# Performance work log

Hardware: AMD Instinct MI355X
Metric: run time of the kernel (lower is better)

The kernel has to match this reference:

```python
import jax, jax.numpy as jnp
import numpy as np


def conv2d(x, w, b):
    # x: [B,C,H,W], w: [O,C,K,K] (VALID, stride 1)
    out = jax.lax.conv_general_dilated(
        x, w, window_strides=(1, 1), padding='VALID',
        dimension_numbers=('NCHW', 'OIHW', 'NCHW'))
    return out + b[None, :, None, None]


def deform_conv2d(x, offset, w, b):
    # torchvision DeformConv2d semantics, offset_groups=1, stride=1, padding=0.
    # x: [B,C,H,W]; offset: [B, 2*K*K, Ho, Wo] with (dy, dx) interleaved per tap.
    B, C, H, W = x.shape
    O, _, K, _ = w.shape
    KK = K * K
    Ho, Wo = H - K + 1, W - K + 1
    off = offset.reshape(B, KK, 2, Ho, Wo)
    ky = (jnp.arange(KK) // K).astype(x.dtype)
    kx = (jnp.arange(KK) % K).astype(x.dtype)
    # sampling positions p0 + p_k + dp  -> [B, KK, Ho, Wo]
    py = ky[None, :, None, None] + jnp.arange(Ho, dtype=x.dtype)[None, None, :, None] + off[:, :, 0]
    px = kx[None, :, None, None] + jnp.arange(Wo, dtype=x.dtype)[None, None, None, :] + off[:, :, 1]
    y0 = jnp.floor(py)
    x0 = jnp.floor(px)
    wy = py - y0  # fractional parts
    wx = px - x0
    y0i = y0.astype(jnp.int32)
    x0i = x0.astype(jnp.int32)

    def corner(yi, xi):
        valid = ((yi >= 0) & (yi < H) & (xi >= 0) & (xi < W)).astype(x.dtype)
        yc = jnp.clip(yi, 0, H - 1)
        xc = jnp.clip(xi, 0, W - 1)
        # per-batch gather over all channels -> [B, C, KK, Ho, Wo]
        g = jax.vmap(lambda im, a, bb: im[:, a, bb])(x, yc, xc)
        return g * valid[:, None]

    v00 = corner(y0i, x0i)
    v01 = corner(y0i, x0i + 1)
    v10 = corner(y0i + 1, x0i)
    v11 = corner(y0i + 1, x0i + 1)
    wy_ = wy[:, None]  # [B,1,KK,Ho,Wo]
    wx_ = wx[:, None]
    samp = (v00 * (1 - wy_) * (1 - wx_) + v01 * (1 - wy_) * wx_
            + v10 * wy_ * (1 - wx_) + v11 * wy_ * wx_)
    out = jnp.einsum('bckhw,ock->bohw', samp, w.reshape(O, C, KK))
    return out + b[None, :, None, None]


_STAGES = [
    # (in_ch, out_ch, K)
    (1, 16, 3), (16, 32, 3), (32, 16, 5), (16, 16, 7), (16, 8, 5), (8, 4, 3),
]


def setup_inputs() -> dict:
    key = jax.random.key(0)
    keys = iter(jax.random.split(key, 64))
    inp = {'x': jax.random.normal(next(keys), (512, 1, 33, 33), dtype=jnp.float32)}
    for i, (ci, co, k) in enumerate(_STAGES, start=1):
        # offset-predicting conv: small init so offsets stay near the regular grid
        inp[f'ow{i}'] = jax.random.normal(next(keys), (2 * k * k, ci, k, k), dtype=jnp.float32) * 0.05
        inp[f'ob{i}'] = jax.random.normal(next(keys), (2 * k * k,), dtype=jnp.float32) * 0.05
        scale = 1.0 / np.sqrt(ci * k * k)
        inp[f'w{i}'] = jax.random.normal(next(keys), (co, ci, k, k), dtype=jnp.float32) * scale
        inp[f'b{i}'] = jax.random.normal(next(keys), (co,), dtype=jnp.float32) * scale
    inp['fc1_w'] = jax.random.normal(next(keys), (256, 13 * 13 * 4), dtype=jnp.float32) * (1.0 / np.sqrt(676))
    inp['fc1_b'] = jnp.zeros((256,), dtype=jnp.float32)
    inp['fc2_w'] = jax.random.normal(next(keys), (10, 256), dtype=jnp.float32) * (1.0 / np.sqrt(256))
    inp['fc2_b'] = jnp.zeros((10,), dtype=jnp.float32)
    return inp


def reference(x, ow1, ob1, w1, b1, ow2, ob2, w2, b2, ow3, ob3, w3, b3,
              ow4, ob4, w4, b4, ow5, ob5, w5, b5, ow6, ob6, w6, b6,
              fc1_w, fc1_b, fc2_w, fc2_b):
    h = jax.nn.relu(deform_conv2d(x, conv2d(x, ow1, ob1), w1, b1))
    h = jax.nn.relu(deform_conv2d(h, conv2d(h, ow2, ob2), w2, b2))
    h = deform_conv2d(h, conv2d(h, ow3, ob3), w3, b3)  # NOTE: no ReLU on stage 3 (matches source)
    h = jax.nn.relu(deform_conv2d(h, conv2d(h, ow4, ob4), w4, b4))
    h = jax.nn.relu(deform_conv2d(h, conv2d(h, ow5, ob5), w5, b5))
    h = jax.nn.relu(deform_conv2d(h, conv2d(h, ow6, ob6), w6, b6))
    flat = h.reshape(h.shape[0], -1)  # [B, 4*13*13]
    z = jax.nn.relu(flat @ fc1_w.T + fc1_b)
    return z @ fc2_w.T + fc2_b
```

## Files before the change

kernel.cpp:

```cpp
#include <hip/hip_runtime.h>

typedef __attribute__((ext_vector_type(8))) short bf16x8;
typedef __attribute__((ext_vector_type(4))) float f32x4;
typedef __attribute__((ext_vector_type(4))) unsigned int u32x4;
typedef unsigned short ushort_t;

__device__ inline ushort_t bf16_trunc(float f) { return (ushort_t)(__float_as_uint(f) >> 16); }
__device__ inline float bf16_to_f(ushort_t u) { return __uint_as_float(((unsigned int)u) << 16); }

__device__ inline unsigned int hi_pair(unsigned int u1, unsigned int u0) {
    return __builtin_amdgcn_perm(u1, u0, 0x07060302u);
}

__device__ inline void split8(const f32x4 sA, const f32x4 sB, bf16x8& ahi, bf16x8& alo)
{
    unsigned int u[8], h[8], d[8];
#pragma unroll
    for (int j = 0; j < 4; ++j) {
        u[j]     = __float_as_uint(sA[j]);
        u[4 + j] = __float_as_uint(sB[j]);
    }
#pragma unroll
    for (int j = 0; j < 8; ++j) {
        h[j] = u[j] & 0xffff0000u;
        d[j] = __float_as_uint(__uint_as_float(u[j]) - __uint_as_float(h[j]));
    }
    union { u32x4 w; bf16x8 v; } H, L;
    H.w = (u32x4){hi_pair(h[1], h[0]), hi_pair(h[3], h[2]), hi_pair(h[5], h[4]), hi_pair(h[7], h[6])};
    L.w = (u32x4){hi_pair(d[1], d[0]), hi_pair(d[3], d[2]), hi_pair(d[5], d[4]), hi_pair(d[7], d[6])};
    ahi = H.v;
    alo = L.v;
}

template<int CI, int KK, int KKPAD, int NPAD, int OC>
__global__ __launch_bounds__(256)
void wprep(const float* __restrict__ w, ushort_t* __restrict__ bhi, ushort_t* __restrict__ blo)
{
    const int idx = blockIdx.x * 256 + threadIdx.x;
    if (idx >= KKPAD * NPAD * CI) return;
    const int kk  = idx / (NPAD * CI);
    const int rem = idx - kk * (NPAD * CI);
    const int n   = rem / CI;
    const int ci  = rem - n * CI;
    const float v = (kk < KK && n < OC) ? w[((size_t)n * CI + ci) * KK + kk] : 0.f;
    const ushort_t h = bf16_trunc(v);
    bhi[idx] = h;
    blo[idx] = bf16_trunc(v - bf16_to_f(h));
}

template<int CI, int KK, int TPAD, int NPAD, int OC>
__global__ __launch_bounds__(256)
void wprep_d(const float* __restrict__ w, ushort_t* __restrict__ bhi, ushort_t* __restrict__ blo)
{
    constexpr int NPASS = (CI + 7) / 8;
    constexpr int TOTAL = NPASS * TPAD * NPAD * 8;
    const int idx = blockIdx.x * 256 + threadIdx.x;
    if (idx >= TOTAL) return;
    const int j     = idx & 7;
    const int n     = (idx >> 3) % NPAD;
    const int kslot = (idx >> 3) / NPAD;
    const int pass  = kslot / TPAD;
    const int tap   = kslot - pass * TPAD;
    const int ci    = pass * 8 + j;
    const float v = (tap < KK && n < OC && ci < CI) ? w[((size_t)n * CI + ci) * KK + tap] : 0.f;
    const ushort_t h = bf16_trunc(v);
    bhi[idx] = h;
    blo[idx] = bf16_trunc(v - bf16_to_f(h));
}

template<int CI, int K, int H, int W, int Ho, int Wo, int OC, int NTTOT, int NT0, int KSTEPS>
__global__ __launch_bounds__(256)
void conv_mfma(const ushort_t* __restrict__ Xhi, const ushort_t* __restrict__ Xlo,
               const ushort_t* __restrict__ Bhi, const ushort_t* __restrict__ Blo,
               const float* __restrict__ bias, float* __restrict__ out, int Mtotal)
{
    constexpr int NPAD = NTTOT * 16;
    constexpr int HW   = H * W;
    constexpr int HoWo = Ho * Wo;
    constexpr int NPASS = CI / 8;
    constexpr int TKS  = 32 / CI;
    constexpr int ROWS = TKS * NT0 * 16;
    constexpr int BSTR = CI + 8;
    constexpr int CH8  = CI / 8;
    constexpr int CHUNKS = ROWS * CH8;

    __shared__ __align__(16) ushort_t sBh[2][ROWS * BSTR];
    __shared__ __align__(16) ushort_t sBl[2][ROWS * BSTR];

    const int tid  = threadIdx.x;
    const int lane = tid & 63;
    const int wid  = tid >> 6;
    const int col  = lane & 15;
    const int quad = lane >> 4;

    const int mBase  = blockIdx.x * 256 + wid * 64;
    const int ntBase = blockIdx.y * NT0;

    int aBase[4];
#pragma unroll
    for (int mt = 0; mt < 4; ++mt) {
        int mm = mBase + mt * 16 + col;
        if (mm >= Mtotal) mm = Mtotal - 1;
        const int b   = mm / HoWo;
        const int pos = mm - b * HoWo;
        const int oy  = pos / Wo;
        const int ox  = pos - oy * Wo;
        aBase[mt] = b * NPASS * HW + oy * W + ox;
    }

    f32x4 acc[4][NT0];
#pragma unroll
    for (int mt = 0; mt < 4; ++mt)
#pragma unroll
        for (int nt = 0; nt < NT0; ++nt) acc[mt][nt] = (f32x4){0.f, 0.f, 0.f, 0.f};

    auto loadSlab = [&](int ks, int buf) {
        const int tap0 = ks * TKS;
        for (int i = tid; i < CHUNKS; i += 256) {
            const int row = i / CH8;
            const int c8  = i - row * CH8;
            const int t   = row / (NT0 * 16);
            const int nn  = row - t * (NT0 * 16);
            int n = ntBase * 16 + nn;
            if (n > NPAD - 1) n = NPAD - 1;
            const int g = ((tap0 + t) * NPAD + n) * CI + c8 * 8;
            *(bf16x8*)(sBh[buf] + row * BSTR + c8 * 8) = *(const bf16x8*)(Bhi + g);
            *(bf16x8*)(sBl[buf] + row * BSTR + c8 * 8) = *(const bf16x8*)(Blo + g);
        }
    };

    loadSlab(0, 0);
    __syncthreads();

#pragma unroll
    for (int ks = 0; ks < KSTEPS; ++ks) {
        if (ks + 1 < KSTEPS) loadSlab(ks + 1, (ks + 1) & 1);

        const int k0   = ks * 32 + quad * 8;
        const int tap  = k0 / CI;
        const int tloc = tap - ks * TKS;
        const int ci   = k0 - tap * CI;
        const int g    = ci >> 3;
        const int dkk  = (tap / K) * W + (tap - (tap / K) * K);

        bf16x8 ah[4], al[4];
#pragma unroll
        for (int mt = 0; mt < 4; ++mt) {
            const size_t aoff = (size_t)(aBase[mt] + g * HW + dkk) * 8;
            ah[mt] = *(const bf16x8*)(Xhi + aoff);
            al[mt] = *(const bf16x8*)(Xlo + aoff);
        }
        const ushort_t* __restrict__ bhp = sBh[ks & 1];
        const ushort_t* __restrict__ blp = sBl[ks & 1];
#pragma unroll
        for (int nt = 0; nt < NT0; ++nt) {
            const int ntg = ntBase + nt;
            if (ntg < NTTOT) {
                const int lrow = ((tloc * NT0 + nt) * 16 + col) * BSTR + ci;
                const bf16x8 bh = *(const bf16x8*)(bhp + lrow);
                const bf16x8 bl = *(const bf16x8*)(blp + lrow);
#pragma unroll
                for (int mt = 0; mt < 4; ++mt) {
                    acc[mt][nt] = __builtin_amdgcn_mfma_f32_16x16x32_bf16(ah[mt], bh, acc[mt][nt], 0, 0, 0);
                    acc[mt][nt] = __builtin_amdgcn_mfma_f32_16x16x32_bf16(al[mt], bh, acc[mt][nt], 0, 0, 0);
                    acc[mt][nt] = __builtin_amdgcn_mfma_f32_16x16x32_bf16(ah[mt], bl, acc[mt][nt], 0, 0, 0);
                }
            }
        }
        __syncthreads();
    }

#pragma unroll
    for (int mt = 0; mt < 4; ++mt) {
#pragma unroll
        for (int nt = 0; nt < NT0; ++nt) {
            const int ntg = ntBase + nt;
            const int n   = ntg * 16 + col;
            if (ntg < NTTOT && n < OC) {
                const float bv = bias[n];
#pragma unroll
                for (int r = 0; r < 4; ++r) {
                    const int m = mBase + mt * 16 + quad * 4 + r;
                    if (m < Mtotal) {
                        const int b   = m / HoWo;
                        const int pos = m - b * HoWo;
                        out[((size_t)b * OC + n) * HoWo + pos] = acc[mt][nt][r] + bv;
                    }
                }
            }
        }
    }
}

template<int K, int CI, int CO, int H, int W, int Ho, int Wo, bool RELU,
         int MT, int TPAD, bool OUTPL>
__global__ __launch_bounds__(MT * 64, 4)
void deform_mfma(const ushort_t* __restrict__ Xhi, const ushort_t* __restrict__ Xlo,
                 const float* __restrict__ off,
                 const ushort_t* __restrict__ Bph, const ushort_t* __restrict__ Bpl,
                 const float* __restrict__ bias,
                 float* __restrict__ outF, ushort_t* __restrict__ oHi, ushort_t* __restrict__ oLo)
{
    static_assert(CI % 16 == 0, "deform_mfma v2 stages 16 channels per pass");
    constexpr int KK     = K * K;
    constexpr int HW     = H * W;
    constexpr int HoWo   = Ho * Wo;
    constexpr int NG8    = CI / 8;
    constexpr int NPASS  = CI / 16;
    constexpr int NPO    = CO / 8;
    constexpr int NT     = (CO + 15) / 16;
    constexpr int NPAD   = NT * 16;
    constexpr int TSTR   = 20;
    constexpr int TG     = TPAD / 4;
    constexpr int nMB    = (HoWo + MT * 16 - 1) / (MT * 16);
    constexpr int THREADS = MT * 64;
    __shared__ __align__(16) float tile[HW * TSTR];

    const int b    = blockIdx.x / nMB;
    const int mb   = blockIdx.x - b * nMB;
    const int tid  = threadIdx.x;
    const int wid  = tid >> 6;
    const int lane = tid & 63;
    const int col  = lane & 15;
    const int quad = lane >> 4;

    const int pixel0 = (mb * MT + wid) * 16;
    const int s      = pixel0 + col;
    const bool am    = (s < HoWo);
    const int oy = s / Wo, ox = s - oy * Wo;

    const float* offB = off + (size_t)b * 2 * KK * HoWo;

    f32x4 acc[NT];
#pragma unroll
    for (int nt = 0; nt < NT; ++nt) acc[nt] = (f32x4){0.f, 0.f, 0.f, 0.f};

    float pw00[TG], pw01[TG], pw10[TG], pw11[TG];
    int   pi00[TG], pi01[TG], pi10[TG], pi11[TG];
    if constexpr (NPASS > 1) {
#pragma unroll
        for (int t = 0; t < TG; ++t) {
            pw00[t] = pw01[t] = pw10[t] = pw11[t] = 0.f;
            pi00[t] = pi01[t] = pi10[t] = pi11[t] = 0;
        }
    }

#pragma unroll
    for (int pass = 0; pass < NPASS; ++pass) {
        __syncthreads();
        for (int pos = tid; pos < HW; pos += THREADS) {
            const size_t gbase = ((size_t)(b * NG8 + pass * 2) * HW + pos) * 8;
            const bf16x8 h0 = *(const bf16x8*)(Xhi + gbase);
            const bf16x8 l0 = *(const bf16x8*)(Xlo + gbase);
            const bf16x8 h1 = *(const bf16x8*)(Xhi + gbase + (size_t)HW * 8);
            const bf16x8 l1 = *(const bf16x8*)(Xlo + gbase + (size_t)HW * 8);
            f32x4 v0, v1, v2, v3;
#pragma unroll
            for (int j = 0; j < 4; ++j) {
                v0[j] = bf16_to_f((ushort_t)h0[j])     + bf16_to_f((ushort_t)l0[j]);
                v1[j] = bf16_to_f((ushort_t)h0[4 + j]) + bf16_to_f((ushort_t)l0[4 + j]);
                v2[j] = bf16_to_f((ushort_t)h1[j])     + bf16_to_f((ushort_t)l1[j]);
                v3[j] = bf16_to_f((ushort_t)h1[4 + j]) + bf16_to_f((ushort_t)l1[4 + j]);
            }
            float* tp = tile + pos * TSTR;
            *(f32x4*)(tp + 0)  = v0;
            *(f32x4*)(tp + 4)  = v1;
            *(f32x4*)(tp + 8)  = v2;
            *(f32x4*)(tp + 12) = v3;
        }
        __syncthreads();

#pragma unroll
        for (int tg = 0; tg < TG; ++tg) {
            const int tap = tg * 4 + quad;

            float w00 = 0.f, w01 = 0.f, w10 = 0.f, w11 = 0.f;
            int   i00 = 0,   i01 = 0,   i10 = 0,   i11 = 0;

            if (pass == 0) {
                if (am && tap < KK) {
                    const float dy = offB[(size_t)(2 * tap + 0) * HoWo + s];
                    const float dx = offB[(size_t)(2 * tap + 1) * HoWo + s];
                    const float py = (float)(tap / K + oy) + dy;
                    const float px = (float)(tap % K + ox) + dx;
                    const float y0f = floorf(py), x0f = floorf(px);
                    const float wy = py - y0f, wx = px - x0f;
                    const int y0 = (int)y0f, x0 = (int)x0f;
                    const int y1 = y0 + 1,   x1 = x0 + 1;

                    const float m00 = (y0 >= 0 && y0 < H && x0 >= 0 && x0 < W) ? 1.f : 0.f;
                    const float m01 = (y0 >= 0 && y0 < H && x1 >= 0 && x1 < W) ? 1.f : 0.f;
                    const float m10 = (y1 >= 0 && y1 < H && x0 >= 0 && x0 < W) ? 1.f : 0.f;
                    const float m11 = (y1 >= 0 && y1 < H && x1 >= 0 && x1 < W) ? 1.f : 0.f;

                    w00 = (1.f - wy) * (1.f - wx) * m00;
                    w01 = (1.f - wy) * wx         * m01;
                    w10 = wy         * (1.f - wx) * m10;
                    w11 = wy         * wx         * m11;

                    const int y0c = min(max(y0, 0), H - 1), y1c = min(max(y1, 0), H - 1);
                    const int x0c = min(max(x0, 0), W - 1), x1c = min(max(x1, 0), W - 1);
                    i00 = (y0c * W + x0c) * TSTR;
                    i01 = (y0c * W + x1c) * TSTR;
                    i10 = (y1c * W + x0c) * TSTR;
                    i11 = (y1c * W + x1c) * TSTR;
                }
                if constexpr (NPASS > 1) {
                    pw00[tg] = w00; pw01[tg] = w01; pw10[tg] = w10; pw11[tg] = w11;
                    pi00[tg] = i00; pi01[tg] = i01; pi10[tg] = i10; pi11[tg] = i11;
                }
            } else if constexpr (NPASS > 1) {
                w00 = pw00[tg]; w01 = pw01[tg]; w10 = pw10[tg]; w11 = pw11[tg];
                i00 = pi00[tg]; i01 = pi01[tg]; i10 = pi10[tg]; i11 = pi11[tg];
            }

#pragma unroll
            for (int g = 0; g < 2; ++g) {
                const float* tp = tile + g * 8;
                const f32x4 a00 = *(const f32x4*)(tp + i00);
                const f32x4 c00 = *(const f32x4*)(tp + i00 + 4);
                const f32x4 a01 = *(const f32x4*)(tp + i01);
                const f32x4 c01 = *(const f32x4*)(tp + i01 + 4);
                const f32x4 a10 = *(const f32x4*)(tp + i10);
                const f32x4 c10 = *(const f32x4*)(tp + i10 + 4);
                const f32x4 a11 = *(const f32x4*)(tp + i11);
                const f32x4 c11 = *(const f32x4*)(tp + i11 + 4);

                f32x4 sA = a00 * w00 + a01 * w01 + a10 * w10 + a11 * w11;
                f32x4 sB = c00 * w00 + c01 * w01 + c10 * w10 + c11 * w11;

                bf16x8 ahi, alo;
                split8(sA, sB, ahi, alo);

                const int kslot = (pass * 2 + g) * TPAD + tap;
#pragma unroll
                for (int nt = 0; nt < NT; ++nt) {
                    const bf16x8 bh = *(const bf16x8*)(Bph + ((size_t)kslot * NPAD + nt * 16 + col) * 8);
                    const bf16x8 bl = *(const bf16x8*)(Bpl + ((size_t)kslot * NPAD + nt * 16 + col) * 8);
                    acc[nt] = __builtin_amdgcn_mfma_f32_16x16x32_bf16(ahi, bh, acc[nt], 0, 0, 0);
                    acc[nt] = __builtin_amdgcn_mfma_f32_16x16x32_bf16(alo, bh, acc[nt], 0, 0, 0);
                    acc[nt] = __builtin_amdgcn_mfma_f32_16x16x32_bf16(ahi, bl, acc[nt], 0, 0, 0);
                }
            }
        }
    }

#pragma unroll
    for (int nt = 0; nt < NT; ++nt) {
        const int n = nt * 16 + col;
        if (n < CO) {
            const float bv = bias[n];
#pragma unroll
            for (int r = 0; r < 4; ++r) {
                const int m = pixel0 + quad * 4 + r;
                if (m < HoWo) {
                    float v = acc[nt][r] + bv;
                    if (RELU) v = fmaxf(v, 0.f);
                    if (OUTPL) {
                        const size_t o = (((size_t)b * NPO + (n >> 3)) * HoWo + m) * 8 + (n & 7);
                        const ushort_t h = bf16_trunc(v);
                        oHi[o] = h;
                        oLo[o] = bf16_trunc(v - bf16_to_f(h));
                    } else {
                        outF[((size_t)b * CO + n) * HoWo + m] = v;
                    }
                }
            }
        }
    }
}

template<int K, int CI, int CO, int H, int W, int Ho, int Wo, bool RELU,
         int CSPLIT, int STRIDE, int THREADS, int SPLIT, bool OUTPL>
__global__ __launch_bounds__(THREADS)
void deform_lds(const float* __restrict__ x, const float* __restrict__ off,
                const float* __restrict__ w, const float* __restrict__ bias,
                float* __restrict__ outF, ushort_t* __restrict__ oHi, ushort_t* __restrict__ oLo)
{
    constexpr int KK    = K * K;
    constexpr int HW    = H * W;
    constexpr int HoWo  = Ho * Wo;
    constexpr int NPASS = CI / CSPLIT;
    constexpr int NPO   = (CO + 7) / 8;
    constexpr int CHUNK = (HoWo + SPLIT - 1) / SPLIT;
    static_assert(CHUNK <= THREADS, "chunk must fit in one block");
    __shared__ __align__(16) float tile[HW * STRIDE];

    const int b   = blockIdx.x / SPLIT;
    const int sp  = blockIdx.x - b * SPLIT;
    const int tid = threadIdx.x;
    const int s   = sp * CHUNK + tid;
    const bool active = (tid < CHUNK) && (s < HoWo);

    const int oy = s / Wo, ox = s - oy * Wo;
    const float* offp = off + ((size_t)b * 2 * KK) * HoWo + s;

    float acc[CO];
#pragma unroll
    for (int o = 0; o < CO; ++o) acc[o] = 0.f;

    for (int pass = 0; pass < NPASS; ++pass) {
        const int cbase = pass * CSPLIT;
        __syncthreads();
        for (int pos = tid; pos < HW; pos += THREADS) {
#pragma unroll
            for (int c = 0; c < CSPLIT; ++c)
                tile[pos * STRIDE + c] = x[((size_t)b * CI + (cbase + c)) * HW + pos];
        }
        __syncthreads();

        if (active) {
            for (int kk = 0; kk < KK; ++kk) {
                const float dy = offp[(size_t)(2 * kk + 0) * HoWo];
                const float dx = offp[(size_t)(2 * kk + 1) * HoWo];
                const float py = (float)(kk / K + oy) + dy;
                const float px = (float)(kk % K + ox) + dx;
                const float y0f = floorf(py), x0f = floorf(px);
                const float wy = py - y0f, wx = px - x0f;
                const int y0 = (int)y0f, x0 = (int)x0f;
                const int y1 = y0 + 1,   x1 = x0 + 1;

                const float m00 = (y0 >= 0 && y0 < H && x0 >= 0 && x0 < W) ? 1.f : 0.f;
                const float m01 = (y0 >= 0 && y0 < H && x1 >= 0 && x1 < W) ? 1.f : 0.f;
                const float m10 = (y1 >= 0 && y1 < H && x0 >= 0 && x0 < W) ? 1.f : 0.f;
                const float m11 = (y1 >= 0 && y1 < H && x1 >= 0 && x1 < W) ? 1.f : 0.f;

                const float w00 = (1.f - wy) * (1.f - wx) * m00;
                const float w01 = (1.f - wy) * wx         * m01;
                const float w10 = wy         * (1.f - wx) * m10;
                const float w11 = wy         * wx         * m11;

                const int y0c = min(max(y0, 0), H - 1), y1c = min(max(y1, 0), H - 1);
                const int x0c = min(max(x0, 0), W - 1), x1c = min(max(x1, 0), W - 1);
                const int i00 = (y0c * W + x0c) * STRIDE;
                const int i01 = (y0c * W + x1c) * STRIDE;
                const int i10 = (y1c * W + x0c) * STRIDE;
                const int i11 = (y1c * W + x1c) * STRIDE;

                if constexpr (CSPLIT % 4 == 0) {
#pragma unroll
                    for (int cg = 0; cg < CSPLIT; cg += 4) {
                        const f32x4 v00 = *(const f32x4*)(tile + i00 + cg);
                        const f32x4 v01 = *(const f32x4*)(tile + i01 + cg);
                        const f32x4 v10 = *(const f32x4*)(tile + i10 + cg);
                        const f32x4 v11 = *(const f32x4*)(tile + i11 + cg);
#pragma unroll
                        for (int j = 0; j < 4; ++j) {
                            const float sv = fmaf(v11[j], w11, fmaf(v10[j], w10,
                                             fmaf(v01[j], w01, v00[j] * w00)));
#pragma unroll
                            for (int o = 0; o < CO; ++o)
                                acc[o] = fmaf(sv, w[(size_t)(o * CI + cbase + cg + j) * KK + kk], acc[o]);
                        }
                    }
                } else {
                    const float sv = fmaf(tile[i11], w11, fmaf(tile[i10], w10,
                                     fmaf(tile[i01], w01, tile[i00] * w00)));
#pragma unroll
                    for (int o = 0; o < CO; ++o)
                        acc[o] = fmaf(sv, w[(size_t)(o * CI + cbase) * KK + kk], acc[o]);
                }
            }
        }
    }

    if (active) {
#pragma unroll
        for (int o = 0; o < CO; ++o) {
            float v = acc[o] + bias[o];
            if (RELU) v = fmaxf(v, 0.f);
            if (OUTPL) {
                const size_t oi = (((size_t)b * NPO + (o >> 3)) * HoWo + s) * 8 + (o & 7);
                const ushort_t h = bf16_trunc(v);
                oHi[oi] = h;
                oLo[oi] = bf16_trunc(v - bf16_to_f(h));
            } else {
                outF[((size_t)b * CO + o) * HoWo + s] = v;
            }
        }
    }
}

template<int K, int CI, int NOC, int OC, int H, int W, int Ho, int Wo, int PIX>
__global__ __launch_bounds__(256)
void conv_tile(const float* __restrict__ x, const float* __restrict__ w,
               const float* __restrict__ bias, float* __restrict__ out)
{
    constexpr int KK   = K * K;
    constexpr int HoWo = Ho * Wo;
    constexpr int WoG  = (Wo + PIX - 1) / PIX;
    constexpr int G    = Ho * WoG;
    constexpr int XV   = PIX + K - 1;

    const int oc0   = blockIdx.y * NOC;
    const int g_all = blockIdx.x * 256 + threadIdx.x;
    const int b     = g_all / G;
    const int g     = g_all - b * G;
    const int oy    = g / WoG;
    const int ox0   = (g - oy * WoG) * PIX;

    const float* xbp = x + (b * CI) * (H * W) + oy * W + ox0;
    const float* wp  = w + oc0 * (CI * KK);

    float acc[PIX][NOC];
#pragma unroll
    for (int p = 0; p < PIX; ++p)
#pragma unroll
        for (int j = 0; j < NOC; ++j) acc[p][j] = bias[oc0 + j];

    const int lim = W - 1 - ox0;

    for (int ci = 0; ci < CI; ++ci) {
        const float* xc = xbp + ci * (H * W);
#pragma unroll
        for (int ky = 0; ky < K; ++ky) {
            float xv[XV];
#pragma unroll
            for (int i = 0; i < XV; ++i) {
                const int off = (i <= lim) ? i : lim;
                xv[i] = xc[ky * W + off];
            }
#pragma unroll
            for (int kx = 0; kx < K; ++kx) {
#pragma unroll
                for (int p = 0; p < PIX; ++p) {
                    const float v = xv[p + kx];
#pragma unroll
                    for (int j = 0; j < NOC; ++j)
                        acc[p][j] = fmaf(v, wp[j * (CI * KK) + ci * KK + ky * K + kx], acc[p][j]);
                }
            }
        }
    }

    float* op = out + (b * OC + oc0) * HoWo + oy * Wo + ox0;
#pragma unroll
    for (int p = 0; p < PIX; ++p) {
        if (ox0 + p < Wo) {
#pragma unroll
            for (int j = 0; j < NOC; ++j) op[j * HoWo + p] = acc[p][j];
        }
    }
}

template<int IN, int OUT>
__global__ __launch_bounds__(256)
void wtrans(const float* __restrict__ w, float* __restrict__ wt)
{
    const int idx = blockIdx.x * 256 + threadIdx.x;
    if (idx >= IN * OUT) return;
    const int i = idx / OUT, j = idx - i * OUT;
    wt[idx] = w[(size_t)j * IN + i];
}

template<int IN, int OUT, bool RELU>
__global__ __launch_bounds__(256)
void fc_t(const float* __restrict__ h, const float* __restrict__ wt,
          const float* __restrict__ bias, float* __restrict__ out, int B)
{
    const int idx = blockIdx.x * 256 + threadIdx.x;
    if (idx >= B * OUT) return;
    const int b = idx / OUT;
    const int j = idx - b * OUT;
    const float* hb = h + (size_t)b * IN;
    float acc = bias[j];
#pragma unroll 4
    for (int i = 0; i < IN; ++i)
        acc = fmaf(hb[i], wt[(size_t)i * OUT + j], acc);
    if (RELU) acc = fmaxf(acc, 0.f);
    out[idx] = acc;
}

extern "C" void kernel_launch(void* const* d_in, const int* in_sizes, int n_in,
                              void* d_out, int out_size, void* d_ws, size_t ws_size,
                              hipStream_t stream)
{
    const int B = 512;
    const float* x = (const float*)d_in[0];
    const float *ow[6], *ob[6], *w[6], *bi[6];
    for (int i = 0; i < 6; ++i) {
        ow[i] = (const float*)d_in[1 + 4 * i];
        ob[i] = (const float*)d_in[2 + 4 * i];
        w[i]  = (const float*)d_in[3 + 4 * i];
        bi[i] = (const float*)d_in[4 + 4 * i];
    }
    const float* fc1w = (const float*)d_in[25];
    const float* fc1b = (const float*)d_in[26];
    const float* fc2w = (const float*)d_in[27];
    const float* fc2b = (const float*)d_in[28];
    float* out = (float*)d_out;

    float* P   = (float*)d_ws;
    float* Q   = P  + 14000000;
    float* OFF = Q  + 14000000;
    float* Z   = OFF + 18200000;
    ushort_t* WBhi = (ushort_t*)(Z + 200000);
    ushort_t* WBlo = WBhi + 200000;
    ushort_t* WDhi = WBlo + 200000;
    ushort_t* WDlo = WDhi + 200000;
    float* WT1 = (float*)(WDlo + 200000);
    float* WT2 = WT1 + 173056;

    const dim3 blk(256);
    #define GRIDT(Ho, Wo, PIX, NG) dim3((B * (Ho) * (((Wo) + (PIX) - 1) / (PIX)) + 255) / 256, (NG), 1)
    #define CEILDIV(a, b) (((a) + (b) - 1) / (b))

    ushort_t* PL2h = (ushort_t*)Q;  ushort_t* PL2l = PL2h + (size_t)(B * 961 + 2048) * 16;
    ushort_t* PL3h = (ushort_t*)P;  ushort_t* PL3l = PL3h + (size_t)(B * 841 + 2048) * 32;
    ushort_t* PL4h = (ushort_t*)Q;  ushort_t* PL4l = PL4h + (size_t)(B * 625 + 2048) * 16;
    ushort_t* PL5h = (ushort_t*)P;  ushort_t* PL5l = PL5h + (size_t)(B * 361 + 2048) * 16;

    conv_tile<3, 1, 6, 18, 33, 33, 31, 31, 4><<<GRIDT(31, 31, 4, 3), blk, 0, stream>>>(x, ow[0], ob[0], OFF);
    deform_lds<3, 1, 16, 33, 33, 31, 31, true, 1, 1, 512, 2, true><<<dim3(B * 2), dim3(512), 0, stream>>>(x, OFF, w[0], bi[0], nullptr, PL2h, PL2l);

    {
        const int Mv = B * 841;
        wprep<16, 9, 10, 32, 18><<<CEILDIV(10 * 32 * 16, 256), blk, 0, stream>>>(ow[1], WBhi, WBlo);
        conv_mfma<16, 3, 31, 31, 29, 29, 18, 2, 2, 5><<<dim3(CEILDIV(Mv, 256), 1), blk, 0, stream>>>(PL2h, PL2l, WBhi, WBlo, ob[1], OFF, Mv);
        wprep_d<16, 9, 12, 32, 32><<<CEILDIV(2 * 12 * 32 * 8, 256), blk, 0, stream>>>(w[1], WDhi, WDlo);
        deform_mfma<3, 16, 32, 31, 31, 29, 29, true, 8, 12, true><<<dim3(B * 7), dim3(512), 0, stream>>>(PL2h, PL2l, OFF, WDhi, WDlo, bi[1], nullptr, PL3h, PL3l);
    }
    {
        const int Mv = B * 625;
        wprep<32, 25, 25, 64, 50><<<CEILDIV(25 * 64 * 32, 256), blk, 0, stream>>>(ow[2], WBhi, WBlo);
        conv_mfma<32, 5, 29, 29, 25, 25, 50, 4, 4, 25><<<dim3(CEILDIV(Mv, 256), 1), blk, 0, stream>>>(PL3h, PL3l, WBhi, WBlo, ob[2], OFF, Mv);
        wprep_d<32, 25, 28, 16, 16><<<CEILDIV(4 * 28 * 16 * 8, 256), blk, 0, stream>>>(w[2], WDhi, WDlo);
        deform_mfma<5, 32, 16, 29, 29, 25, 25, false, 8, 28, true><<<dim3(B * 5), dim3(512), 0, stream>>>(PL3h, PL3l, OFF, WDhi, WDlo, bi[2], nullptr, PL4h, PL4l);
    }
    {
        const int Mv = B * 361;
        wprep<16, 49, 50, 112, 98><<<CEILDIV(50 * 112 * 16, 256), blk, 0, stream>>>(ow[3], WBhi, WBlo);
        conv_mfma<16, 7, 25, 25, 19, 19, 98, 7, 4, 25><<<dim3(CEILDIV(Mv, 256), 2), blk, 0, stream>>>(PL4h, PL4l, WBhi, WBlo, ob[3], OFF, Mv);
        wprep_d<16, 49, 52, 16, 16><<<CEILDIV(2 * 52 * 16 * 8, 256), blk, 0, stream>>>(w[3], WDhi, WDlo);
        deform_mfma<7, 16, 16, 25, 25, 19, 19, true, 8, 52, true><<<dim3(B * 3), dim3(512), 0, stream>>>(PL4h, PL4l, OFF, WDhi, WDlo, bi[3], nullptr, PL5h, PL5l);
    }
    {
        const int Mv = B * 225;
        wprep<16, 25, 26, 64, 50><<<CEILDIV(26 * 64 * 16, 256), blk, 0, stream>>>(ow[4], WBhi, WBlo);
        conv_mfma<16, 5, 19, 19, 15, 15, 50, 4, 4, 13><<<dim3(CEILDIV(Mv, 256), 1), blk, 0, stream>>>(PL5h, PL5l, WBhi, WBlo, ob[4], OFF, Mv);
        wprep_d<16, 25, 28, 16, 8><<<CEILDIV(2 * 28 * 16 * 8, 256), blk, 0, stream>>>(w[4], WDhi, WDlo);
        deform_mfma<5, 16, 8, 19, 19, 15, 15, true, 4, 28, false><<<dim3(B * 4), dim3(256), 0, stream>>>(PL5h, PL5l, OFF, WDhi, WDlo, bi[4], Q, nullptr, nullptr);
    }
    conv_tile<3, 8, 6, 18, 15, 15, 13, 13, 4><<<GRIDT(13, 13, 4, 3), blk, 0, stream>>>(Q, ow[5], ob[5], OFF);
    deform_lds<3, 8, 4, 15, 15, 13, 13, true, 8, 12, 192, 1, false><<<dim3(B), dim3(192), 0, stream>>>(Q, OFF, w[5], bi[5], P, nullptr, nullptr);

    wtrans<676, 256><<<CEILDIV(676 * 256, 256), blk, 0, stream>>>(fc1w, WT1);
    wtrans<256, 10><<<CEILDIV(256 * 10, 256), blk, 0, stream>>>(fc2w, WT2);
    fc_t<676, 256, true><<<dim3(CEILDIV(B * 256, 256)), blk, 0, stream>>>(P, WT1, fc1b, Z, B);
    fc_t<256, 10, false><<<dim3(CEILDIV(B * 10, 256)), blk, 0, stream>>>(Z, WT2, fc2b, out, B);

    #undef GRIDT
    #undef CEILDIV
}
```

Measured before the change: 866.8 us.

## Stage all input channels in LDS at once in deform_mfma

```diff
diff --git a/kernel.cpp b/kernel.cpp
--- a/kernel.cpp
+++ b/kernel.cpp
@@ -201,16 +201,15 @@
                  const float* __restrict__ bias,
                  float* __restrict__ outF, ushort_t* __restrict__ oHi, ushort_t* __restrict__ oLo)
 {
-    static_assert(CI % 16 == 0, "deform_mfma v2 stages 16 channels per pass");
+    static_assert(CI % 8 == 0, "channel-grouped layout requires CI % 8 == 0");
     constexpr int KK     = K * K;
     constexpr int HW     = H * W;
     constexpr int HoWo   = Ho * Wo;
-    constexpr int NG8    = CI / 8;
-    constexpr int NPASS  = CI / 16;
+    constexpr int GP     = CI / 8;
     constexpr int NPO    = CO / 8;
     constexpr int NT     = (CO + 15) / 16;
     constexpr int NPAD   = NT * 16;
-    constexpr int TSTR   = 20;
+    constexpr int TSTR   = CI + 4;
     constexpr int TG     = TPAD / 4;
     constexpr int nMB    = (HoWo + MT * 16 - 1) / (MT * 16);
     constexpr int THREADS = MT * 64;
@@ -235,112 +234,86 @@
 #pragma unroll
     for (int nt = 0; nt < NT; ++nt) acc[nt] = (f32x4){0.f, 0.f, 0.f, 0.f};
 
-    float pw00[TG], pw01[TG], pw10[TG], pw11[TG];
-    int   pi00[TG], pi01[TG], pi10[TG], pi11[TG];
-    if constexpr (NPASS > 1) {
-#pragma unroll
-        for (int t = 0; t < TG; ++t) {
-            pw00[t] = pw01[t] = pw10[t] = pw11[t] = 0.f;
-            pi00[t] = pi01[t] = pi10[t] = pi11[t] = 0;
-        }
-    }
-
-#pragma unroll
-    for (int pass = 0; pass < NPASS; ++pass) {
-        __syncthreads();
-        for (int pos = tid; pos < HW; pos += THREADS) {
-            const size_t gbase = ((size_t)(b * NG8 + pass * 2) * HW + pos) * 8;
-            const bf16x8 h0 = *(const bf16x8*)(Xhi + gbase);
-            const bf16x8 l0 = *(const bf16x8*)(Xlo + gbase);
-            const bf16x8 h1 = *(const bf16x8*)(Xhi + gbase + (size_t)HW * 8);
-            const bf16x8 l1 = *(const bf16x8*)(Xlo + gbase + (size_t)HW * 8);
-            f32x4 v0, v1, v2, v3;
+    for (int pos = tid; pos < HW; pos += THREADS) {
+        float* tp = tile + pos * TSTR;
+#pragma unroll
+        for (int g = 0; g < GP; ++g) {
+            const size_t gbase = ((size_t)(b * GP + g) * HW + pos) * 8;
+            const bf16x8 h8 = *(const bf16x8*)(Xhi + gbase);
+            const bf16x8 l8 = *(const bf16x8*)(Xlo + gbase);
+            f32x4 vA, vB;
 #pragma unroll
             for (int j = 0; j < 4; ++j) {
-                v0[j] = bf16_to_f((ushort_t)h0[j])     + bf16_to_f((ushort_t)l0[j]);
-                v1[j] = bf16_to_f((ushort_t)h0[4 + j]) + bf16_to_f((ushort_t)l0[4 + j]);
-                v2[j] = bf16_to_f((ushort_t)h1[j])     + bf16_to_f((ushort_t)l1[j]);
-                v3[j] = bf16_to_f((ushort_t)h1[4 + j]) + bf16_to_f((ushort_t)l1[4 + j]);
-            }
-            float* tp = tile + pos * TSTR;
-            *(f32x4*)(tp + 0)  = v0;
-            *(f32x4*)(tp + 4)  = v1;
-            *(f32x4*)(tp + 8)  = v2;
-            *(f32x4*)(tp + 12) = v3;
-        }
-        __syncthreads();
-
-#pragma unroll
-        for (int tg = 0; tg < TG; ++tg) {
-            const int tap = tg * 4 + quad;
-
-            float w00 = 0.f, w01 = 0.f, w10 = 0.f, w11 = 0.f;
-            int   i00 = 0,   i01 = 0,   i10 = 0,   i11 = 0;
-
-            if (pass == 0) {
-                if (am && tap < KK) {
-                    const float dy = offB[(size_t)(2 * tap + 0) * HoWo + s];
-                    const float dx = offB[(size_t)(2 * tap + 1) * HoWo + s];
-                    const float py = (float)(tap / K + oy) + dy;
-                    const float px = (float)(tap % K + ox) + dx;
-                    const float y0f = floorf(py), x0f = floorf(px);
-                    const float wy = py - y0f, wx = px - x0f;
-                    const int y0 = (int)y0f, x0 = (int)x0f;
-                    const int y1 = y0 + 1,   x1 = x0 + 1;
-
-                    const float m00 = (y0 >= 0 && y0 < H && x0 >= 0 && x0 < W) ? 1.f : 0.f;
-                    const float m01 = (y0 >= 0 && y0 < H && x1 >= 0 && x1 < W) ? 1.f : 0.f;
-                    const float m10 = (y1 >= 0 && y1 < H && x0 >= 0 && x0 < W) ? 1.f : 0.f;
-                    const float m11 = (y1 >= 0 && y1 < H && x1 >= 0 && x1 < W) ? 1.f : 0.f;
-
-                    w00 = (1.f - wy) * (1.f - wx) * m00;
-                    w01 = (1.f - wy) * wx         * m01;
-                    w10 = wy         * (1.f - wx) * m10;
-                    w11 = wy         * wx         * m11;
-
-                    const int y0c = min(max(y0, 0), H - 1), y1c = min(max(y1, 0), H - 1);
-                    const int x0c = min(max(x0, 0), W - 1), x1c = min(max(x1, 0), W - 1);
-                    i00 = (y0c * W + x0c) * TSTR;
-                    i01 = (y0c * W + x1c) * TSTR;
-                    i10 = (y1c * W + x0c) * TSTR;
-                    i11 = (y1c * W + x1c) * TSTR;
-                }
-                if constexpr (NPASS > 1) {
-                    pw00[tg] = w00; pw01[tg] = w01; pw10[tg] = w10; pw11[tg] = w11;
-                    pi00[tg] = i00; pi01[tg] = i01; pi10[tg] = i10; pi11[tg] = i11;
-                }
-            } else if constexpr (NPASS > 1) {
-                w00 = pw00[tg]; w01 = pw01[tg]; w10 = pw10[tg]; w11 = pw11[tg];
-                i00 = pi00[tg]; i01 = pi01[tg]; i10 = pi10[tg]; i11 = pi11[tg];
-            }
-
-#pragma unroll
-            for (int g = 0; g < 2; ++g) {
-                const float* tp = tile + g * 8;
-                const f32x4 a00 = *(const f32x4*)(tp + i00);
-                const f32x4 c00 = *(const f32x4*)(tp + i00 + 4);
-                const f32x4 a01 = *(const f32x4*)(tp + i01);
-                const f32x4 c01 = *(const f32x4*)(tp + i01 + 4);
-                const f32x4 a10 = *(const f32x4*)(tp + i10);
-                const f32x4 c10 = *(const f32x4*)(tp + i10 + 4);
-                const f32x4 a11 = *(const f32x4*)(tp + i11);
-                const f32x4 c11 = *(const f32x4*)(tp + i11 + 4);
-
-                f32x4 sA = a00 * w00 + a01 * w01 + a10 * w10 + a11 * w11;
-                f32x4 sB = c00 * w00 + c01 * w01 + c10 * w10 + c11 * w11;
-
-                bf16x8 ahi, alo;
-                split8(sA, sB, ahi, alo);
-
-                const int kslot = (pass * 2 + g) * TPAD + tap;
-#pragma unroll
-                for (int nt = 0; nt < NT; ++nt) {
-                    const bf16x8 bh = *(const bf16x8*)(Bph + ((size_t)kslot * NPAD + nt * 16 + col) * 8);
-                    const bf16x8 bl = *(const bf16x8*)(Bpl + ((size_t)kslot * NPAD + nt * 16 + col) * 8);
-                    acc[nt] = __builtin_amdgcn_mfma_f32_16x16x32_bf16(ahi, bh, acc[nt], 0, 0, 0);
-                    acc[nt] = __builtin_amdgcn_mfma_f32_16x16x32_bf16(alo, bh, acc[nt], 0, 0, 0);
-                    acc[nt] = __builtin_amdgcn_mfma_f32_16x16x32_bf16(ahi, bl, acc[nt], 0, 0, 0);
-                }
+                vA[j] = bf16_to_f((ushort_t)h8[j])     + bf16_to_f((ushort_t)l8[j]);
+                vB[j] = bf16_to_f((ushort_t)h8[4 + j]) + bf16_to_f((ushort_t)l8[4 + j]);
+            }
+            *(f32x4*)(tp + g * 8)     = vA;
+            *(f32x4*)(tp + g * 8 + 4) = vB;
+        }
+    }
+    __syncthreads();
+
+#pragma unroll
+    for (int tg = 0; tg < TG; ++tg) {
+        const int tap = tg * 4 + quad;
+
+        float w00 = 0.f, w01 = 0.f, w10 = 0.f, w11 = 0.f;
+        int   i00 = 0,   i01 = 0,   i10 = 0,   i11 = 0;
+
+        if (am && tap < KK) {
+            const float dy = offB[(size_t)(2 * tap + 0) * HoWo + s];
+            const float dx = offB[(size_t)(2 * tap + 1) * HoWo + s];
+            const float py = (float)(tap / K + oy) + dy;
+            const float px = (float)(tap % K + ox) + dx;
+            const float y0f = floorf(py), x0f = floorf(px);
+            const float wy = py - y0f, wx = px - x0f;
+            const int y0 = (int)y0f, x0 = (int)x0f;
+            const int y1 = y0 + 1,   x1 = x0 + 1;
+
+            const float m00 = (y0 >= 0 && y0 < H && x0 >= 0 && x0 < W) ? 1.f : 0.f;
+            const float m01 = (y0 >= 0 && y0 < H && x1 >= 0 && x1 < W) ? 1.f : 0.f;
+            const float m10 = (y1 >= 0 && y1 < H && x0 >= 0 && x0 < W) ? 1.f : 0.f;
+            const float m11 = (y1 >= 0 && y1 < H && x1 >= 0 && x1 < W) ? 1.f : 0.f;
+
+            w00 = (1.f - wy) * (1.f - wx) * m00;
+            w01 = (1.f - wy) * wx         * m01;
+            w10 = wy         * (1.f - wx) * m10;
+            w11 = wy         * wx         * m11;
+
+            const int y0c = min(max(y0, 0), H - 1), y1c = min(max(y1, 0), H - 1);
+            const int x0c = min(max(x0, 0), W - 1), x1c = min(max(x1, 0), W - 1);
+            i00 = (y0c * W + x0c) * TSTR;
+            i01 = (y0c * W + x1c) * TSTR;
+            i10 = (y1c * W + x0c) * TSTR;
+            i11 = (y1c * W + x1c) * TSTR;
+        }
+
+#pragma unroll
+        for (int g = 0; g < GP; ++g) {
+            const float* tp = tile + g * 8;
+            const f32x4 a00 = *(const f32x4*)(tp + i00);
+            const f32x4 c00 = *(const f32x4*)(tp + i00 + 4);
+            const f32x4 a01 = *(const f32x4*)(tp + i01);
+            const f32x4 c01 = *(const f32x4*)(tp + i01 + 4);
+            const f32x4 a10 = *(const f32x4*)(tp + i10);
+            const f32x4 c10 = *(const f32x4*)(tp + i10 + 4);
+            const f32x4 a11 = *(const f32x4*)(tp + i11);
+            const f32x4 c11 = *(const f32x4*)(tp + i11 + 4);
+
+            f32x4 sA = a00 * w00 + a01 * w01 + a10 * w10 + a11 * w11;
+            f32x4 sB = c00 * w00 + c01 * w01 + c10 * w10 + c11 * w11;
+
+            bf16x8 ahi, alo;
+            split8(sA, sB, ahi, alo);
+
+            const int kslot = g * TPAD + tap;
+#pragma unroll
+            for (int nt = 0; nt < NT; ++nt) {
+                const bf16x8 bh = *(const bf16x8*)(Bph + ((size_t)kslot * NPAD + nt * 16 + col) * 8);
+                const bf16x8 bl = *(const bf16x8*)(Bpl + ((size_t)kslot * NPAD + nt * 16 + col) * 8);
+                acc[nt] = __builtin_amdgcn_mfma_f32_16x16x32_bf16(ahi, bh, acc[nt], 0, 0, 0);
+                acc[nt] = __builtin_amdgcn_mfma_f32_16x16x32_bf16(alo, bh, acc[nt], 0, 0, 0);
+                acc[nt] = __builtin_amdgcn_mfma_f32_16x16x32_bf16(ahi, bl, acc[nt], 0, 0, 0);
             }
         }
     }
@@ -625,7 +598,7 @@
         wprep<32, 25, 25, 64, 50><<<CEILDIV(25 * 64 * 32, 256), blk, 0, stream>>>(ow[2], WBhi, WBlo);
         conv_mfma<32, 5, 29, 29, 25, 25, 50, 4, 4, 25><<<dim3(CEILDIV(Mv, 256), 1), blk, 0, stream>>>(PL3h, PL3l, WBhi, WBlo, ob[2], OFF, Mv);
         wprep_d<32, 25, 28, 16, 16><<<CEILDIV(4 * 28 * 16 * 8, 256), blk, 0, stream>>>(w[2], WDhi, WDlo);
-        deform_mfma<5, 32, 16, 29, 29, 25, 25, false, 8, 28, true><<<dim3(B * 5), dim3(512), 0, stream>>>(PL3h, PL3l, OFF, WDhi, WDlo, bi[2], nullptr, PL4h, PL4l);
+        deform_mfma<5, 32, 16, 29, 29, 25, 25, false, 14, 28, true><<<dim3(B * 3), dim3(896), 0, stream>>>(PL3h, PL3l, OFF, WDhi, WDlo, bi[2], nullptr, PL4h, PL4l);
     }
     {
         const int Mv = B * 361;
```

Result: faster. 837.3 us (-3.4%).
